# Kernel tuning notes

Hardware: AMD Instinct MI355X
Metric: run time of the kernel (lower is better)

The kernel has to match this reference:

```python
import jax, jax.numpy as jnp
import numpy as np

USER_NUM = 1_000_000
ITEM_NUM = 100_000
N_FEATS = 8
DICT_SIZE = 10_000
VEC_DIM = 16
K = 32
BATCH = 16_384
TOTAL_DIM = (2 + N_FEATS) * VEC_DIM  # 160


def setup_inputs() -> dict:
    key = jax.random.key(0)
    ks = jax.random.split(key, 7)
    inputs = jax.random.randint(ks[0], (BATCH, 2 + N_FEATS), 0, DICT_SIZE, dtype=jnp.int32)
    user_table = jax.random.normal(ks[1], (USER_NUM, VEC_DIM), dtype=jnp.float32) * 0.05
    item_table = jax.random.normal(ks[2], (ITEM_NUM, VEC_DIM), dtype=jnp.float32) * 0.05
    feat_tables = jax.random.normal(ks[3], (N_FEATS, DICT_SIZE, VEC_DIM), dtype=jnp.float32) * 0.05
    w = jax.random.normal(ks[4], (TOTAL_DIM, 1), dtype=jnp.float32) * 0.05
    b = jnp.zeros((1,), dtype=jnp.float32)
    k_mat = jax.random.normal(ks[5], (TOTAL_DIM, K), dtype=jnp.float32) * (1.0 / np.sqrt(TOTAL_DIM))
    return {"inputs": inputs, "user_table": user_table, "item_table": item_table,
            "feat_tables": feat_tables, "w": w, "b": b, "k_mat": k_mat}


def reference(inputs, user_table, item_table, feat_tables, w, b, k_mat):
    B = inputs.shape[0]
    user_vec = user_table[inputs[:, 0]]            # [B, D]
    item_vec = item_table[inputs[:, 1]]            # [B, D]
    # gather each feature table with its own id column: [F, B, D]
    feat_vecs = jax.vmap(lambda tbl, idx: tbl[idx], in_axes=(0, 1))(feat_tables, inputs[:, 2:])
    feat_flat = jnp.transpose(feat_vecs, (1, 0, 2)).reshape(B, -1)  # [B, F*D]
    x = jnp.concatenate([user_vec, item_vec, feat_flat], axis=1)    # [B, total_dim]
    linear = x @ w + b                                              # [B, 1]
    inter_1 = jnp.square(x @ k_mat)                                 # [B, K]
    inter_2 = jnp.square(x) @ jnp.square(k_mat)                     # [B, K]
    cross = 0.5 * jnp.sum(inter_1 - inter_2, axis=1, keepdims=True) # [B, 1]
    return jax.nn.sigmoid(linear + cross)
```

## Files before the change

kernel.cpp:

```cpp
#include <hip/hip_runtime.h>
#include <math.h>

#define NFEAT 10
#define DICT 10000

typedef __attribute__((ext_vector_type(8))) short bf16x8;
typedef __attribute__((ext_vector_type(4))) float f32x4;
typedef __attribute__((ext_vector_type(4))) unsigned u32x4;

__device__ inline unsigned short f2bf(float f) {
    unsigned u = __builtin_bit_cast(unsigned, f);
    u += 0x7FFFu + ((u >> 16) & 1u);
    return (unsigned short)(u >> 16);
}
__device__ inline unsigned cvt2(float lo, float hi) {
    return (unsigned)f2bf(lo) | ((unsigned)f2bf(hi) << 16);
}

__global__ __launch_bounds__(256) void fm_fused(
    const int* __restrict__ inputs,
    const float* __restrict__ user_table,
    const float* __restrict__ item_table,
    const float* __restrict__ feat_tables,
    const float* __restrict__ wvec,
    const float* __restrict__ bb,
    const float* __restrict__ k_mat,
    float* __restrict__ out)
{
    const int tid  = threadIdx.x;
    const int lane = tid & 63;
    const int gwid = blockIdx.x * 4 + (tid >> 6);
    const int col  = lane & 15;
    const int kg   = lane >> 4;
    const int e    = gwid * 16 + col;
    const int fsel = kg >> 1;
    const int hoff = (kg & 1) * 8;

    int idx[5];
    #pragma unroll
    for (int c = 0; c < 5; ++c)
        idx[c] = inputs[e * NFEAT + 2 * c + fsel];

    float4 u0[5], u1[5];
    #pragma unroll
    for (int c = 0; c < 5; ++c) {
        const float* tbl = (c == 0)
            ? (fsel ? item_table : user_table)
            : (feat_tables + (size_t)(2 * c + fsel - 2) * (DICT * 16));
        const float* src = tbl + (size_t)idx[c] * 16 + hoff;
        u0[c] = *(const float4*)src;
        u1[c] = *(const float4*)(src + 4);
    }

    bf16x8 bk0[5], bk1[5], bq0[5], bq1[5];
    #pragma unroll
    for (int c = 0; c < 5; ++c) {
        const int dbase = c * 32 + kg * 8;
        float f0[8], f1[8];
        #pragma unroll
        for (int j = 0; j < 8; ++j) {
            f0[j] = k_mat[(dbase + j) * 32 + col];
            f1[j] = k_mat[(dbase + j) * 32 + 16 + col];
        }
        u32x4 p0, p1, q0, q1;
        #pragma unroll
        for (int j = 0; j < 4; ++j) {
            p0[j] = cvt2(f0[2*j],          f0[2*j+1]);
            p1[j] = cvt2(f1[2*j],          f1[2*j+1]);
            q0[j] = cvt2(f0[2*j]*f0[2*j],  f0[2*j+1]*f0[2*j+1]);
            q1[j] = cvt2(f1[2*j]*f1[2*j],  f1[2*j+1]*f1[2*j+1]);
        }
        bk0[c] = __builtin_bit_cast(bf16x8, p0);
        bk1[c] = __builtin_bit_cast(bf16x8, p1);
        bq0[c] = __builtin_bit_cast(bf16x8, q0);
        bq1[c] = __builtin_bit_cast(bf16x8, q1);
    }

    float lin = 0.f;
    #pragma unroll
    for (int c = 0; c < 5; ++c) {
        const int dbase = c * 32 + kg * 8;
        float4 w0 = *(const float4*)&wvec[dbase];
        float4 w1 = *(const float4*)&wvec[dbase + 4];
        lin = fmaf(u0[c].x, w0.x, lin); lin = fmaf(u0[c].y, w0.y, lin);
        lin = fmaf(u0[c].z, w0.z, lin); lin = fmaf(u0[c].w, w0.w, lin);
        lin = fmaf(u1[c].x, w1.x, lin); lin = fmaf(u1[c].y, w1.y, lin);
        lin = fmaf(u1[c].z, w1.z, lin); lin = fmaf(u1[c].w, w1.w, lin);
    }
    lin += __shfl_xor(lin, 16, 64);
    lin += __shfl_xor(lin, 32, 64);

    f32x4 acc0  = {0,0,0,0};
    f32x4 acc1  = {0,0,0,0};
    f32x4 accT0 = {0,0,0,0};
    f32x4 accT1 = {0,0,0,0};
    #pragma unroll
    for (int c = 0; c < 5; ++c) {
        u32x4 pa, pa2;
        pa[0]  = cvt2(u0[c].x, u0[c].y);  pa[1]  = cvt2(u0[c].z, u0[c].w);
        pa[2]  = cvt2(u1[c].x, u1[c].y);  pa[3]  = cvt2(u1[c].z, u1[c].w);
        pa2[0] = cvt2(u0[c].x*u0[c].x, u0[c].y*u0[c].y);
        pa2[1] = cvt2(u0[c].z*u0[c].z, u0[c].w*u0[c].w);
        pa2[2] = cvt2(u1[c].x*u1[c].x, u1[c].y*u1[c].y);
        pa2[3] = cvt2(u1[c].z*u1[c].z, u1[c].w*u1[c].w);
        bf16x8 a  = __builtin_bit_cast(bf16x8, pa);
        bf16x8 a2 = __builtin_bit_cast(bf16x8, pa2);
        acc0  = __builtin_amdgcn_mfma_f32_16x16x32_bf16(a,  bk0[c], acc0,  0, 0, 0);
        acc1  = __builtin_amdgcn_mfma_f32_16x16x32_bf16(a,  bk1[c], acc1,  0, 0, 0);
        accT0 = __builtin_amdgcn_mfma_f32_16x16x32_bf16(a2, bq0[c], accT0, 0, 0, 0);
        accT1 = __builtin_amdgcn_mfma_f32_16x16x32_bf16(a2, bq1[c], accT1, 0, 0, 0);
    }

    const float bval = bb[0];
    #pragma unroll
    for (int r = 0; r < 4; ++r) {
        float v = acc0[r]*acc0[r] + acc1[r]*acc1[r] - accT0[r] - accT1[r];
        #pragma unroll
        for (int m = 1; m <= 8; m <<= 1)
            v += __shfl_xor(v, m, 64);
        float lm = __shfl(lin, kg * 4 + r, 64);
        if (col == 0) {
            float z = lm + bval + 0.5f * v;
            out[gwid * 16 + kg * 4 + r] = 1.0f / (1.0f + __expf(-z));
        }
    }
}

extern "C" void kernel_launch(void* const* d_in, const int* in_sizes, int n_in,
                              void* d_out, int out_size, void* d_ws, size_t ws_size,
                              hipStream_t stream) {
    const int*   inputs      = (const int*)  d_in[0];
    const float* user_table  = (const float*)d_in[1];
    const float* item_table  = (const float*)d_in[2];
    const float* feat_tables = (const float*)d_in[3];
    const float* w           = (const float*)d_in[4];
    const float* b           = (const float*)d_in[5];
    const float* k_mat       = (const float*)d_in[6];
    float* out = (float*)d_out;

    int nblocks = out_size / 64;
    fm_fused<<<nblocks, 256, 0, stream>>>(inputs, user_table, item_table,
                                          feat_tables, w, b, k_mat, out);
}
```

Before: 12.04 us.

## Split linear and squared MFMA paths across wave pairs with LDS reduction

```diff
diff --git a/kernel.cpp b/kernel.cpp
--- a/kernel.cpp
+++ b/kernel.cpp
@@ -1,4 +1,5 @@
 #include <hip/hip_runtime.h>
+#include <hip/hip_bf16.h>
 #include <math.h>
 
 #define NFEAT 10
@@ -9,15 +10,16 @@
 typedef __attribute__((ext_vector_type(4))) unsigned u32x4;
 
 __device__ inline unsigned short f2bf(float f) {
-    unsigned u = __builtin_bit_cast(unsigned, f);
-    u += 0x7FFFu + ((u >> 16) & 1u);
-    return (unsigned short)(u >> 16);
+    __hip_bfloat16 h = __float2bfloat16(f);
+    unsigned short s;
+    __builtin_memcpy(&s, &h, sizeof(s));
+    return s;
 }
 __device__ inline unsigned cvt2(float lo, float hi) {
     return (unsigned)f2bf(lo) | ((unsigned)f2bf(hi) << 16);
 }
 
-__global__ __launch_bounds__(256) void fm_fused(
+__global__ __launch_bounds__(256, 2) void fm_fused(
     const int* __restrict__ inputs,
     const float* __restrict__ user_table,
     const float* __restrict__ item_table,
@@ -27,14 +29,19 @@
     const float* __restrict__ k_mat,
     float* __restrict__ out)
 {
-    const int tid  = threadIdx.x;
-    const int lane = tid & 63;
-    const int gwid = blockIdx.x * 4 + (tid >> 6);
-    const int col  = lane & 15;
-    const int kg   = lane >> 4;
-    const int e    = gwid * 16 + col;
-    const int fsel = kg >> 1;
-    const int hoff = (kg & 1) * 8;
+    __shared__ float part_t[2][16];
+
+    const int tid   = threadIdx.x;
+    const int lane  = tid & 63;
+    const int wid   = tid >> 6;
+    const int tile  = wid >> 1;
+    const bool sq   = (wid & 1) != 0;
+    const int gtile = blockIdx.x * 2 + tile;
+    const int col   = lane & 15;
+    const int kg    = lane >> 4;
+    const int e     = gtile * 16 + col;
+    const int fsel  = kg >> 1;
+    const int hoff  = (kg & 1) * 8;
 
     int idx[5];
     #pragma unroll
@@ -52,7 +59,7 @@
         u1[c] = *(const float4*)(src + 4);
     }
 
-    bf16x8 bk0[5], bk1[5], bq0[5], bq1[5];
+    bf16x8 b0[5], b1[5];
     #pragma unroll
     for (int c = 0; c < 5; ++c) {
         const int dbase = c * 32 + kg * 8;
@@ -62,66 +69,75 @@
             f0[j] = k_mat[(dbase + j) * 32 + col];
             f1[j] = k_mat[(dbase + j) * 32 + 16 + col];
         }
-        u32x4 p0, p1, q0, q1;
+        if (sq) {
+            #pragma unroll
+            for (int j = 0; j < 8; ++j) { f0[j] *= f0[j]; f1[j] *= f1[j]; }
+        }
+        u32x4 p0, p1;
         #pragma unroll
         for (int j = 0; j < 4; ++j) {
-            p0[j] = cvt2(f0[2*j],          f0[2*j+1]);
-            p1[j] = cvt2(f1[2*j],          f1[2*j+1]);
-            q0[j] = cvt2(f0[2*j]*f0[2*j],  f0[2*j+1]*f0[2*j+1]);
-            q1[j] = cvt2(f1[2*j]*f1[2*j],  f1[2*j+1]*f1[2*j+1]);
+            p0[j] = cvt2(f0[2*j], f0[2*j+1]);
+            p1[j] = cvt2(f1[2*j], f1[2*j+1]);
         }
-        bk0[c] = __builtin_bit_cast(bf16x8, p0);
-        bk1[c] = __builtin_bit_cast(bf16x8, p1);
-        bq0[c] = __builtin_bit_cast(bf16x8, q0);
-        bq1[c] = __builtin_bit_cast(bf16x8, q1);
+        b0[c] = __builtin_bit_cast(bf16x8, p0);
+        b1[c] = __builtin_bit_cast(bf16x8, p1);
+    }
+
+    f32x4 acc0 = {0,0,0,0};
+    f32x4 acc1 = {0,0,0,0};
+    #pragma unroll
+    for (int c = 0; c < 5; ++c) {
+        float4 v0 = u0[c], v1 = u1[c];
+        if (sq) {
+            v0.x *= v0.x; v0.y *= v0.y; v0.z *= v0.z; v0.w *= v0.w;
+            v1.x *= v1.x; v1.y *= v1.y; v1.z *= v1.z; v1.w *= v1.w;
+        }
+        u32x4 p;
+        p[0] = cvt2(v0.x, v0.y); p[1] = cvt2(v0.z, v0.w);
+        p[2] = cvt2(v1.x, v1.y); p[3] = cvt2(v1.z, v1.w);
+        bf16x8 a = __builtin_bit_cast(bf16x8, p);
+        acc0 = __builtin_amdgcn_mfma_f32_16x16x32_bf16(a, b0[c], acc0, 0, 0, 0);
+        acc1 = __builtin_amdgcn_mfma_f32_16x16x32_bf16(a, b1[c], acc1, 0, 0, 0);
     }
 
     float lin = 0.f;
-    #pragma unroll
-    for (int c = 0; c < 5; ++c) {
-        const int dbase = c * 32 + kg * 8;
-        float4 w0 = *(const float4*)&wvec[dbase];
-        float4 w1 = *(const float4*)&wvec[dbase + 4];
-        lin = fmaf(u0[c].x, w0.x, lin); lin = fmaf(u0[c].y, w0.y, lin);
-        lin = fmaf(u0[c].z, w0.z, lin); lin = fmaf(u0[c].w, w0.w, lin);
-        lin = fmaf(u1[c].x, w1.x, lin); lin = fmaf(u1[c].y, w1.y, lin);
-        lin = fmaf(u1[c].z, w1.z, lin); lin = fmaf(u1[c].w, w1.w, lin);
-    }
-    lin += __shfl_xor(lin, 16, 64);
-    lin += __shfl_xor(lin, 32, 64);
-
-    f32x4 acc0  = {0,0,0,0};
-    f32x4 acc1  = {0,0,0,0};
-    f32x4 accT0 = {0,0,0,0};
-    f32x4 accT1 = {0,0,0,0};
-    #pragma unroll
-    for (int c = 0; c < 5; ++c) {
-        u32x4 pa, pa2;
-        pa[0]  = cvt2(u0[c].x, u0[c].y);  pa[1]  = cvt2(u0[c].z, u0[c].w);
-        pa[2]  = cvt2(u1[c].x, u1[c].y);  pa[3]  = cvt2(u1[c].z, u1[c].w);
-        pa2[0] = cvt2(u0[c].x*u0[c].x, u0[c].y*u0[c].y);
-        pa2[1] = cvt2(u0[c].z*u0[c].z, u0[c].w*u0[c].w);
-        pa2[2] = cvt2(u1[c].x*u1[c].x, u1[c].y*u1[c].y);
-        pa2[3] = cvt2(u1[c].z*u1[c].z, u1[c].w*u1[c].w);
-        bf16x8 a  = __builtin_bit_cast(bf16x8, pa);
-        bf16x8 a2 = __builtin_bit_cast(bf16x8, pa2);
-        acc0  = __builtin_amdgcn_mfma_f32_16x16x32_bf16(a,  bk0[c], acc0,  0, 0, 0);
-        acc1  = __builtin_amdgcn_mfma_f32_16x16x32_bf16(a,  bk1[c], acc1,  0, 0, 0);
-        accT0 = __builtin_amdgcn_mfma_f32_16x16x32_bf16(a2, bq0[c], accT0, 0, 0, 0);
-        accT1 = __builtin_amdgcn_mfma_f32_16x16x32_bf16(a2, bq1[c], accT1, 0, 0, 0);
+    if (!sq) {
+        #pragma unroll
+        for (int c = 0; c < 5; ++c) {
+            const int dbase = c * 32 + kg * 8;
+            float4 w0 = *(const float4*)&wvec[dbase];
+            float4 w1 = *(const float4*)&wvec[dbase + 4];
+            lin = fmaf(u0[c].x, w0.x, lin); lin = fmaf(u0[c].y, w0.y, lin);
+            lin = fmaf(u0[c].z, w0.z, lin); lin = fmaf(u0[c].w, w0.w, lin);
+            lin = fmaf(u1[c].x, w1.x, lin); lin = fmaf(u1[c].y, w1.y, lin);
+            lin = fmaf(u1[c].z, w1.z, lin); lin = fmaf(u1[c].w, w1.w, lin);
+        }
+        lin += __shfl_xor(lin, 16, 64);
+        lin += __shfl_xor(lin, 32, 64);
     }
 
-    const float bval = bb[0];
+    float sv[4];
     #pragma unroll
     for (int r = 0; r < 4; ++r) {
-        float v = acc0[r]*acc0[r] + acc1[r]*acc1[r] - accT0[r] - accT1[r];
+        float v = sq ? (acc0[r] + acc1[r])
+                     : (acc0[r]*acc0[r] + acc1[r]*acc1[r]);
         #pragma unroll
         for (int m = 1; m <= 8; m <<= 1)
             v += __shfl_xor(v, m, 64);
-        float lm = __shfl(lin, kg * 4 + r, 64);
-        if (col == 0) {
-            float z = lm + bval + 0.5f * v;
-            out[gwid * 16 + kg * 4 + r] = 1.0f / (1.0f + __expf(-z));
+        sv[r] = v;
+        if (sq && col == 0) part_t[tile][kg * 4 + r] = v;
+    }
+    __syncthreads();
+
+    if (!sq) {
+        const float bval = bb[0];
+        #pragma unroll
+        for (int r = 0; r < 4; ++r) {
+            float lm = __shfl(lin, kg * 4 + r, 64);
+            if (col == 0) {
+                float z = lm + bval + 0.5f * (sv[r] - part_t[tile][kg * 4 + r]);
+                out[gtile * 16 + kg * 4 + r] = 1.0f / (1.0f + __expf(-z));
+            }
         }
     }
 }
@@ -138,7 +154,7 @@
     const float* k_mat       = (const float*)d_in[6];
     float* out = (float*)d_out;
 
-    int nblocks = out_size / 64;
+    int nblocks = out_size / 32;
     fm_fused<<<nblocks, 256, 0, stream>>>(inputs, user_table, item_table,
                                           feat_tables, w, b, k_mat, out);
 }
```

New measurement: 11.81 us. Within noise of the previous version (-1.9%).

## Collapse squared-term matmul into a per-feature dot with precomputed row norms

Applied to the files above, without the earlier changes.

```diff
diff --git a/kernel.cpp b/kernel.cpp
--- a/kernel.cpp
+++ b/kernel.cpp
@@ -1,17 +1,20 @@
 #include <hip/hip_runtime.h>
+#include <hip/hip_bf16.h>
 #include <math.h>
 
 #define NFEAT 10
 #define DICT 10000
+#define KP32 84
 
 typedef __attribute__((ext_vector_type(8))) short bf16x8;
 typedef __attribute__((ext_vector_type(4))) float f32x4;
 typedef __attribute__((ext_vector_type(4))) unsigned u32x4;
 
 __device__ inline unsigned short f2bf(float f) {
-    unsigned u = __builtin_bit_cast(unsigned, f);
-    u += 0x7FFFu + ((u >> 16) & 1u);
-    return (unsigned short)(u >> 16);
+    __hip_bfloat16 h = __float2bfloat16(f);
+    unsigned short s;
+    __builtin_memcpy(&s, &h, sizeof(s));
+    return s;
 }
 __device__ inline unsigned cvt2(float lo, float hi) {
     return (unsigned)f2bf(lo) | ((unsigned)f2bf(hi) << 16);
@@ -27,12 +30,16 @@
     const float* __restrict__ k_mat,
     float* __restrict__ out)
 {
+    __shared__ unsigned ldsK32[32 * KP32];
+    __shared__ float    kk2s[160];
+
     const int tid  = threadIdx.x;
     const int lane = tid & 63;
-    const int gwid = blockIdx.x * 4 + (tid >> 6);
+    const int wid  = tid >> 6;
+    const int tile = blockIdx.x * 4 + wid;
     const int col  = lane & 15;
     const int kg   = lane >> 4;
-    const int e    = gwid * 16 + col;
+    const int e    = tile * 16 + col;
     const int fsel = kg >> 1;
     const int hoff = (kg & 1) * 8;
 
@@ -52,76 +59,82 @@
         u1[c] = *(const float4*)(src + 4);
     }
 
-    bf16x8 bk0[5], bk1[5], bq0[5], bq1[5];
+    #pragma unroll
+    for (int u = 0; u < 10; ++u) {
+        int i  = tid + 256 * u;
+        int k  = i / 80;
+        int d2 = i - k * 80;
+        float flo = k_mat[(2 * d2)     * 32 + k];
+        float fhi = k_mat[(2 * d2 + 1) * 32 + k];
+        ldsK32[k * KP32 + d2] = cvt2(flo, fhi);
+    }
+    if (tid < 160) {
+        const float4* row = (const float4*)(k_mat + tid * 32);
+        float acc = 0.f;
+        #pragma unroll
+        for (int u = 0; u < 8; ++u) {
+            float4 v = row[u];
+            acc = fmaf(v.x, v.x, acc); acc = fmaf(v.y, v.y, acc);
+            acc = fmaf(v.z, v.z, acc); acc = fmaf(v.w, v.w, acc);
+        }
+        kk2s[tid] = acc;
+    }
+    __syncthreads();
+
+    const unsigned short* ldsK16 = (const unsigned short*)ldsK32;
+
+    bf16x8 b0[5], b1[5];
     #pragma unroll
     for (int c = 0; c < 5; ++c) {
         const int dbase = c * 32 + kg * 8;
-        float f0[8], f1[8];
-        #pragma unroll
-        for (int j = 0; j < 8; ++j) {
-            f0[j] = k_mat[(dbase + j) * 32 + col];
-            f1[j] = k_mat[(dbase + j) * 32 + 16 + col];
-        }
-        u32x4 p0, p1, q0, q1;
-        #pragma unroll
-        for (int j = 0; j < 4; ++j) {
-            p0[j] = cvt2(f0[2*j],          f0[2*j+1]);
-            p1[j] = cvt2(f1[2*j],          f1[2*j+1]);
-            q0[j] = cvt2(f0[2*j]*f0[2*j],  f0[2*j+1]*f0[2*j+1]);
-            q1[j] = cvt2(f1[2*j]*f1[2*j],  f1[2*j+1]*f1[2*j+1]);
-        }
-        bk0[c] = __builtin_bit_cast(bf16x8, p0);
-        bk1[c] = __builtin_bit_cast(bf16x8, p1);
-        bq0[c] = __builtin_bit_cast(bf16x8, q0);
-        bq1[c] = __builtin_bit_cast(bf16x8, q1);
+        b0[c] = *(const bf16x8*)&ldsK16[(col)      * (2 * KP32) + dbase];
+        b1[c] = *(const bf16x8*)&ldsK16[(col + 16) * (2 * KP32) + dbase];
     }
 
-    float lin = 0.f;
+    f32x4 acc0 = {0,0,0,0};
+    f32x4 acc1 = {0,0,0,0};
+    float lin = 0.f, tq = 0.f;
     #pragma unroll
     for (int c = 0; c < 5; ++c) {
         const int dbase = c * 32 + kg * 8;
+        u32x4 p;
+        p[0] = cvt2(u0[c].x, u0[c].y); p[1] = cvt2(u0[c].z, u0[c].w);
+        p[2] = cvt2(u1[c].x, u1[c].y); p[3] = cvt2(u1[c].z, u1[c].w);
+        bf16x8 a = __builtin_bit_cast(bf16x8, p);
+        acc0 = __builtin_amdgcn_mfma_f32_16x16x32_bf16(a, b0[c], acc0, 0, 0, 0);
+        acc1 = __builtin_amdgcn_mfma_f32_16x16x32_bf16(a, b1[c], acc1, 0, 0, 0);
+
         float4 w0 = *(const float4*)&wvec[dbase];
         float4 w1 = *(const float4*)&wvec[dbase + 4];
+        f32x4  q0 = *(const f32x4*)&kk2s[dbase];
+        f32x4  q1 = *(const f32x4*)&kk2s[dbase + 4];
         lin = fmaf(u0[c].x, w0.x, lin); lin = fmaf(u0[c].y, w0.y, lin);
         lin = fmaf(u0[c].z, w0.z, lin); lin = fmaf(u0[c].w, w0.w, lin);
         lin = fmaf(u1[c].x, w1.x, lin); lin = fmaf(u1[c].y, w1.y, lin);
         lin = fmaf(u1[c].z, w1.z, lin); lin = fmaf(u1[c].w, w1.w, lin);
+        tq = fmaf(u0[c].x*u0[c].x, q0[0], tq); tq = fmaf(u0[c].y*u0[c].y, q0[1], tq);
+        tq = fmaf(u0[c].z*u0[c].z, q0[2], tq); tq = fmaf(u0[c].w*u0[c].w, q0[3], tq);
+        tq = fmaf(u1[c].x*u1[c].x, q1[0], tq); tq = fmaf(u1[c].y*u1[c].y, q1[1], tq);
+        tq = fmaf(u1[c].z*u1[c].z, q1[2], tq); tq = fmaf(u1[c].w*u1[c].w, q1[3], tq);
     }
+
     lin += __shfl_xor(lin, 16, 64);
     lin += __shfl_xor(lin, 32, 64);
-
-    f32x4 acc0  = {0,0,0,0};
-    f32x4 acc1  = {0,0,0,0};
-    f32x4 accT0 = {0,0,0,0};
-    f32x4 accT1 = {0,0,0,0};
-    #pragma unroll
-    for (int c = 0; c < 5; ++c) {
-        u32x4 pa, pa2;
-        pa[0]  = cvt2(u0[c].x, u0[c].y);  pa[1]  = cvt2(u0[c].z, u0[c].w);
-        pa[2]  = cvt2(u1[c].x, u1[c].y);  pa[3]  = cvt2(u1[c].z, u1[c].w);
-        pa2[0] = cvt2(u0[c].x*u0[c].x, u0[c].y*u0[c].y);
-        pa2[1] = cvt2(u0[c].z*u0[c].z, u0[c].w*u0[c].w);
-        pa2[2] = cvt2(u1[c].x*u1[c].x, u1[c].y*u1[c].y);
-        pa2[3] = cvt2(u1[c].z*u1[c].z, u1[c].w*u1[c].w);
-        bf16x8 a  = __builtin_bit_cast(bf16x8, pa);
-        bf16x8 a2 = __builtin_bit_cast(bf16x8, pa2);
-        acc0  = __builtin_amdgcn_mfma_f32_16x16x32_bf16(a,  bk0[c], acc0,  0, 0, 0);
-        acc1  = __builtin_amdgcn_mfma_f32_16x16x32_bf16(a,  bk1[c], acc1,  0, 0, 0);
-        accT0 = __builtin_amdgcn_mfma_f32_16x16x32_bf16(a2, bq0[c], accT0, 0, 0, 0);
-        accT1 = __builtin_amdgcn_mfma_f32_16x16x32_bf16(a2, bq1[c], accT1, 0, 0, 0);
-    }
+    tq  += __shfl_xor(tq, 16, 64);
+    tq  += __shfl_xor(tq, 32, 64);
 
     const float bval = bb[0];
     #pragma unroll
     for (int r = 0; r < 4; ++r) {
-        float v = acc0[r]*acc0[r] + acc1[r]*acc1[r] - accT0[r] - accT1[r];
+        float v = acc0[r]*acc0[r] + acc1[r]*acc1[r];
         #pragma unroll
         for (int m = 1; m <= 8; m <<= 1)
             v += __shfl_xor(v, m, 64);
         float lm = __shfl(lin, kg * 4 + r, 64);
+        float tm = __shfl(tq,  kg * 4 + r, 64);
         if (col == 0) {
-            float z = lm + bval + 0.5f * v;
-            out[gwid * 16 + kg * 4 + r] = 1.0f / (1.0f + __expf(-z));
+            float z = lm + bval + 0.5f * (v - tm);
+            out[tile * 16 + kg * 4 + r] = 1.0f / (1.0f + __expf(-z));
         }
     }
 }
```

Result: faster. 11.67 us (-3.1%).
